# Kernel optimization log

Hardware: AMD Instinct MI355X
Metric: run time of the kernel (lower is better)

The kernel has to match this reference:

```python
import jax, jax.numpy as jnp
import numpy as np

EMB = 1024
HEADS = 16
HEAD_DIM = EMB // HEADS
EPS = 1e-5


def gelu_tanh(x):
    c = jnp.sqrt(jnp.asarray(2.0 / jnp.pi, x.dtype))
    return 0.5 * x * (1.0 + jnp.tanh(c * (x + 0.044715 * x ** 3)))


def layernorm(x, scale, shift):
    mean = jnp.mean(x, axis=-1, keepdims=True)
    var = jnp.mean((x - mean) ** 2, axis=-1, keepdims=True)  # unbiased=False
    return scale * (x - mean) / jnp.sqrt(var + EPS) + shift


def setup_inputs() -> dict:
    key = jax.random.key(0)
    ks = jax.random.split(key, 12)
    d, dff = EMB, 4 * EMB
    sd = 1.0 / np.sqrt(d)
    inp = {
        "x": jax.random.normal(ks[0], (2, 2048, d), jnp.float32),
        "Wq": jax.random.normal(ks[1], (d, d), jnp.float32) * sd,
        "Wk": jax.random.normal(ks[2], (d, d), jnp.float32) * sd,
        "Wv": jax.random.normal(ks[3], (d, d), jnp.float32) * sd,
        "Wo": jax.random.normal(ks[4], (d, d), jnp.float32) * sd,
        "bo": jnp.zeros((d,), jnp.float32),
        "W1": jax.random.normal(ks[5], (d, dff), jnp.float32) * sd,
        "b1": jnp.zeros((dff,), jnp.float32),
        "W2": jax.random.normal(ks[6], (dff, d), jnp.float32) * (1.0 / np.sqrt(dff)),
        "b2": jnp.zeros((d,), jnp.float32),
        "g1": jnp.ones((d,), jnp.float32),
        "s1": jnp.zeros((d,), jnp.float32),
        "g2": jnp.ones((d,), jnp.float32),
        "s2": jnp.zeros((d,), jnp.float32),
    }
    return inp


def attention(x, Wq, Wk, Wv, Wo, bo):
    b, s, d = x.shape
    def heads(W):
        return (x @ W).reshape(b, s, HEADS, HEAD_DIM).transpose(0, 2, 1, 3)  # b h s hd
    q, k, v = heads(Wq), heads(Wk), heads(Wv)
    scores = jnp.einsum("bhqd,bhkd->bhqk", q, k)
    causal = jnp.tril(jnp.ones((s, s), bool))
    scores = jnp.where(causal, scores, -jnp.inf)
    w = jax.nn.softmax(scores / np.sqrt(HEAD_DIM), axis=-1)
    ctx = jnp.einsum("bhqk,bhkd->bqhd", w, v).reshape(b, s, d)
    return ctx @ Wo + bo


def reference(x, Wq, Wk, Wv, Wo, bo, W1, b1, W2, b2, g1, s1, g2, s2):
    h = x + attention(layernorm(x, g1, s1), Wq, Wk, Wv, Wo, bo)
    y = layernorm(h, g2, s2)
    y = gelu_tanh(y @ W1 + b1) @ W2 + b2
    return h + y
```

## Files before the change

kernel.cpp:

```cpp
#include <hip/hip_runtime.h>
#include <hip/hip_bf16.h>
#include <stdint.h>
#include <math.h>

#define EMB   1024
#define DFF   4096
#define HEADS 16
#define HD    64
#define BATCH 2
#define SEQ   2048
#define ROWS  (BATCH * SEQ)

typedef __hip_bfloat16 bf16;
typedef short bf16x8_t __attribute__((ext_vector_type(8)));
typedef float f32x4_t __attribute__((ext_vector_type(4)));

typedef const uint32_t __attribute__((address_space(1)))* gp_t;
typedef uint32_t __attribute__((address_space(3)))* lp_t;

__device__ __forceinline__ void async_copy16(const bf16* g, short* l) {
    __builtin_amdgcn_global_load_lds((gp_t)(const void*)g, (lp_t)(void*)l, 16, 0, 0);
}

__device__ __forceinline__ void wait_lds() {
    __asm__ volatile("" ::: "memory");
    __builtin_amdgcn_s_waitcnt(0xC07F);
    __asm__ volatile("" ::: "memory");
}

__device__ __forceinline__ float gelu_f(float x) {
    float z = 0.7978845608028654f * (x + 0.044715f * x * x * x);
    float e = __builtin_amdgcn_exp2f(z * 2.885390081777927f);
    float t = 1.0f - 2.0f * __builtin_amdgcn_rcpf(e + 1.0f);
    return 0.5f * x * (1.0f + t);
}

__device__ __forceinline__ short bf16_bits(float x) {
    bf16 b = (bf16)x;
    short s;
    __builtin_memcpy(&s, &b, 2);
    return s;
}

__device__ __forceinline__ bf16x8_t load8(const bf16* p) {
    bf16x8_t v;
    __builtin_memcpy(&v, p, 16);
    return v;
}

template<int EPI, int BM>
__global__ __launch_bounds__(256) void gemm_k(
    const bf16* __restrict__ A, const bf16* __restrict__ BT,
    bf16* __restrict__ outB, float* __restrict__ outF,
    const float* __restrict__ bias, const float* __restrict__ resF,
    int N, int K, size_t bStrideZ, size_t cStrideZ)
{
    __shared__ alignas(16) short As[2][BM * 32];
    __shared__ alignas(16) short Bs[2][128 * 32];
    constexpr int AI  = BM / 32;
    constexpr int AIS = BM / 64;
    const int tid  = threadIdx.x;
    const int wave = tid >> 6;
    const int lane = tid & 63;
    const int quad = lane >> 4;
    const int l16  = lane & 15;
    const int m0 = blockIdx.y * BM;
    const int n0 = blockIdx.x * 128;
    const int wm = (wave >> 1) * (BM / 2);
    const int wn = (wave & 1) * 64;

    const bf16* Bz = BT + (size_t)blockIdx.z * bStrideZ;

    const bf16* Ag[AIS]; int aoff[AIS];
    const bf16* Bg[2];   int boff[2];
    #pragma unroll
    for (int i = 0; i < AIS; i++) {
        const int c = i * 256 + tid;
        const int row = c >> 2;
        const int lch = (c & 3) ^ ((row >> 1) & 3);
        Ag[i]   = A + (size_t)(m0 + row) * K + lch * 8;
        aoff[i] = (i * 256 + wave * 64) * 8;
    }
    #pragma unroll
    for (int i = 0; i < 2; i++) {
        const int c = i * 256 + tid;
        const int row = c >> 2;
        const int lch = (c & 3) ^ ((row >> 1) & 3);
        Bg[i]   = Bz + (size_t)(n0 + row) * K + lch * 8;
        boff[i] = (i * 256 + wave * 64) * 8;
    }

    f32x4_t acc[AI][4] = {};

    #pragma unroll
    for (int i = 0; i < AIS; i++) async_copy16(Ag[i], &As[0][aoff[i]]);
    #pragma unroll
    for (int i = 0; i < 2; i++)   async_copy16(Bg[i], &Bs[0][boff[i]]);
    __syncthreads();

    int cur = 0;
    for (int k0 = 0; k0 < K; k0 += 32) {
        const int kn = k0 + 32;
        if (kn < K) {
            #pragma unroll
            for (int i = 0; i < AIS; i++) async_copy16(Ag[i] + kn, &As[cur ^ 1][aoff[i]]);
            #pragma unroll
            for (int i = 0; i < 2; i++)   async_copy16(Bg[i] + kn, &Bs[cur ^ 1][boff[i]]);
        }
        bf16x8_t a[AI], b[4];
        #pragma unroll
        for (int i = 0; i < AI; i++) {
            const int r = wm + i * 16 + l16;
            a[i] = *(const bf16x8_t*)&As[cur][r * 32 + ((quad ^ ((r >> 1) & 3)) << 3)];
        }
        #pragma unroll
        for (int j = 0; j < 4; j++) {
            const int r = wn + j * 16 + l16;
            b[j] = *(const bf16x8_t*)&Bs[cur][r * 32 + ((quad ^ ((r >> 1) & 3)) << 3)];
        }
        #pragma unroll
        for (int i = 0; i < AI; i++)
            #pragma unroll
            for (int j = 0; j < 4; j++)
                acc[i][j] = __builtin_amdgcn_mfma_f32_16x16x32_bf16(
                    a[i], b[j], acc[i][j], 0, 0, 0);
        __syncthreads();
        cur ^= 1;
    }

    bf16* outBz = (EPI == 0) ? outB + (size_t)blockIdx.z * cStrideZ : outB;
    #pragma unroll
    for (int j = 0; j < 4; j++) {
        const int col = n0 + wn + j * 16 + l16;
        float bv = 0.0f;
        if constexpr (EPI != 0) bv = bias[col];
        #pragma unroll
        for (int i = 0; i < AI; i++) {
            #pragma unroll
            for (int r = 0; r < 4; r++) {
                const int row = m0 + wm + i * 16 + quad * 4 + r;
                float v = acc[i][j][r] + bv;
                if constexpr (EPI == 1 || EPI == 3) {
                    v += resF[(size_t)row * N + col];
                    outF[(size_t)row * N + col] = v;
                } else if constexpr (EPI == 2) {
                    outBz[(size_t)row * N + col] = (bf16)gelu_f(v);
                } else {
                    outBz[(size_t)row * N + col] = (bf16)v;
                }
            }
        }
    }
}

__global__ __launch_bounds__(256) void ln_k(
    const float* __restrict__ x, const float* __restrict__ g,
    const float* __restrict__ s, bf16* __restrict__ out)
{
    const int row = blockIdx.x;
    const int t = threadIdx.x;
    const size_t base = (size_t)row * EMB + t * 4;
    float v[4];
    #pragma unroll
    for (int e = 0; e < 4; e++) v[e] = x[base + e];
    float sum = v[0] + v[1] + v[2] + v[3];
    float sq  = v[0]*v[0] + v[1]*v[1] + v[2]*v[2] + v[3]*v[3];
    #pragma unroll
    for (int o = 1; o < 64; o <<= 1) {
        sum += __shfl_xor(sum, o);
        sq  += __shfl_xor(sq, o);
    }
    __shared__ float ssum[4], ssq[4];
    const int wave = t >> 6;
    if ((t & 63) == 0) { ssum[wave] = sum; ssq[wave] = sq; }
    __syncthreads();
    sum = ssum[0] + ssum[1] + ssum[2] + ssum[3];
    sq  = ssq[0] + ssq[1] + ssq[2] + ssq[3];
    const float mean = sum * (1.0f / EMB);
    const float var  = sq * (1.0f / EMB) - mean * mean;
    const float rstd = rsqrtf(var + 1e-5f);
    #pragma unroll
    for (int e = 0; e < 4; e++)
        out[base + e] = (bf16)(g[t * 4 + e] * (v[e] - mean) * rstd + s[t * 4 + e]);
}

template<typename T>
__global__ __launch_bounds__(256) void transpose_k(
    const T* __restrict__ src, bf16* __restrict__ dst, int R, int C)
{
    __shared__ bf16 tile[64][65];
    const size_t bo = (size_t)blockIdx.z * R * C;
    const int tx = threadIdx.x, ty = threadIdx.y;
    const int r0 = blockIdx.y * 64, c0 = blockIdx.x * 64;
    #pragma unroll
    for (int i = 0; i < 16; i++) {
        int r = ty + i * 4;
        tile[r][tx] = (bf16)(float)src[bo + (size_t)(r0 + r) * C + c0 + tx];
    }
    __syncthreads();
    #pragma unroll
    for (int i = 0; i < 16; i++) {
        int c = ty + i * 4;
        dst[bo + (size_t)(c0 + c) * R + r0 + tx] = tile[tx][c];
    }
}

__global__ __launch_bounds__(256) void transpose3_k(
    const float* __restrict__ s0, const float* __restrict__ s1,
    const float* __restrict__ s2, bf16* __restrict__ dst, int R, int C)
{
    __shared__ bf16 tile[64][65];
    const float* src = blockIdx.z == 0 ? s0 : (blockIdx.z == 1 ? s1 : s2);
    bf16* d = dst + (size_t)blockIdx.z * R * C;
    const int tx = threadIdx.x, ty = threadIdx.y;
    const int r0 = blockIdx.y * 64, c0 = blockIdx.x * 64;
    #pragma unroll
    for (int i = 0; i < 16; i++) {
        int r = ty + i * 4;
        tile[r][tx] = (bf16)src[(size_t)(r0 + r) * C + c0 + tx];
    }
    __syncthreads();
    #pragma unroll
    for (int i = 0; i < 16; i++) {
        int c = ty + i * 4;
        d[(size_t)(c0 + c) * R + r0 + tx] = tile[tx][c];
    }
}

__global__ __launch_bounds__(256) void attn_k(
    const bf16* __restrict__ q, const bf16* __restrict__ k,
    const bf16* __restrict__ vt, bf16* __restrict__ ctx)
{
    __shared__ alignas(16) short Ks[2][64 * 64];
    __shared__ alignas(16) short Vs[2][64 * 64];
    __shared__ alignas(16) short P[4][16 * 40];
    const int tid = threadIdx.x;
    const int wv = tid >> 6;
    const int lane = tid & 63;
    const int quad = lane >> 4, l16 = lane & 15;

    const int fid = (int)blockIdx.x;
    const int lid = (fid & 7) * 128 + (fid >> 3);
    const int chunk = 31 - (lid & 31);
    const int h = (lid >> 5) & 15;
    const int b = lid >> 9;
    const size_t rowBase = (size_t)b * SEQ;
    const int qb = chunk * 64 + wv * 16;
    const int NK = chunk + 1;

    const bf16* kcol  = k + rowBase * EMB + h * HD;
    const bf16* vbase = vt + (size_t)(b * HEADS + h) * HD * SEQ;

    bf16x8_t aq[2];
    #pragma unroll
    for (int s2 = 0; s2 < 2; s2++)
        aq[s2] = load8(&q[(rowBase + qb + l16) * EMB + h * HD + s2 * 32 + quad * 8]);

    f32x4_t O[4] = {};
    float l_p[4] = {};

    int krw[2], kgc[2];
    #pragma unroll
    for (int i = 0; i < 2; i++) {
        const int c = i * 256 + tid;
        krw[i] = c >> 3;
        kgc[i] = (c & 7) ^ (krw[i] & 7);
    }
    const int ldsOff[2] = { (0 * 256 + wv * 64) * 8, (1 * 256 + wv * 64) * 8 };

    #pragma unroll
    for (int i = 0; i < 2; i++) {
        async_copy16(kcol + (size_t)krw[i] * EMB + kgc[i] * 8, &Ks[0][ldsOff[i]]);
        async_copy16(vbase + (size_t)krw[i] * SEQ + kgc[i] * 8, &Vs[0][ldsOff[i]]);
    }
    __syncthreads();

    constexpr float SC = 0.125f * 1.44269504088896f;

    int cur = 0;
    for (int kb = 0; kb < NK; ++kb) {
        const int kbase = kb * 64;
        if (kb + 1 < NK) {
            const int nb = kbase + 64;
            #pragma unroll
            for (int i = 0; i < 2; i++) {
                async_copy16(kcol + (size_t)(nb + krw[i]) * EMB + kgc[i] * 8,
                             &Ks[cur ^ 1][ldsOff[i]]);
                async_copy16(vbase + (size_t)krw[i] * SEQ + nb + kgc[i] * 8,
                             &Vs[cur ^ 1][ldsOff[i]]);
            }
        }
        bf16x8_t ck[4][2];
        #pragma unroll
        for (int nt = 0; nt < 4; nt++) {
            const int kr = nt * 16 + l16;
            #pragma unroll
            for (int s2 = 0; s2 < 2; s2++)
                ck[nt][s2] = *(const bf16x8_t*)
                    &Ks[cur][kr * 64 + (((s2 * 4 + quad) ^ (kr & 7)) << 3)];
        }
        f32x4_t sc[4] = {};
        #pragma unroll
        for (int nt = 0; nt < 4; nt++)
            #pragma unroll
            for (int s2 = 0; s2 < 2; s2++)
                sc[nt] = __builtin_amdgcn_mfma_f32_16x16x32_bf16(
                    aq[s2], ck[nt][s2], sc[nt], 0, 0, 0);

        short* Pw = P[wv];
        const bool full = (kbase + 63 <= qb);
        #pragma unroll
        for (int hf = 0; hf < 2; hf++) {
            bf16x8_t cv[4];
            #pragma unroll
            for (int c = 0; c < 4; c++) {
                const int vr = c * 16 + l16;
                cv[c] = *(const bf16x8_t*)
                    &Vs[cur][vr * 64 + (((hf * 4 + quad) ^ (vr & 7)) << 3)];
            }
            if (full) {
                #pragma unroll
                for (int nt2 = 0; nt2 < 2; nt2++) {
                    const int nt = hf * 2 + nt2;
                    #pragma unroll
                    for (int r = 0; r < 4; r++) {
                        const float p = __builtin_amdgcn_exp2f(sc[nt][r] * SC);
                        l_p[r] += p;
                        Pw[(quad * 4 + r) * 40 + nt2 * 16 + l16] = bf16_bits(p);
                    }
                }
            } else {
                #pragma unroll
                for (int nt2 = 0; nt2 < 2; nt2++) {
                    const int nt = hf * 2 + nt2;
                    const int kk = kbase + nt * 16 + l16;
                    #pragma unroll
                    for (int r = 0; r < 4; r++) {
                        const int qg = qb + quad * 4 + r;
                        float s = sc[nt][r] * SC;
                        if (kk > qg) s = -1e30f;
                        const float p = __builtin_amdgcn_exp2f(s);
                        l_p[r] += p;
                        Pw[(quad * 4 + r) * 40 + nt2 * 16 + l16] = bf16_bits(p);
                    }
                }
            }
            wait_lds();
            bf16x8_t pa = *(const bf16x8_t*)&Pw[l16 * 40 + quad * 8];
            #pragma unroll
            for (int c = 0; c < 4; c++)
                O[c] = __builtin_amdgcn_mfma_f32_16x16x32_bf16(pa, cv[c], O[c], 0, 0, 0);
        }
        __syncthreads();
        cur ^= 1;
    }

    #pragma unroll
    for (int r = 0; r < 4; r++) {
        float l = l_p[r];
        l += __shfl_xor(l, 1);
        l += __shfl_xor(l, 2);
        l += __shfl_xor(l, 4);
        l += __shfl_xor(l, 8);
        const float inv = 1.0f / l;
        #pragma unroll
        for (int c = 0; c < 4; c++)
            ctx[(rowBase + qb + quad * 4 + r) * EMB + h * HD + c * 16 + l16]
                = (bf16)(O[c][r] * inv);
    }
}

extern "C" void kernel_launch(void* const* d_in, const int* in_sizes, int n_in,
                              void* d_out, int out_size, void* d_ws, size_t ws_size,
                              hipStream_t stream) {
    const float* X  = (const float*)d_in[0];
    const float* Wq = (const float*)d_in[1];
    const float* Wk = (const float*)d_in[2];
    const float* Wv = (const float*)d_in[3];
    const float* Wo = (const float*)d_in[4];
    const float* bo = (const float*)d_in[5];
    const float* W1 = (const float*)d_in[6];
    const float* b1 = (const float*)d_in[7];
    const float* W2 = (const float*)d_in[8];
    const float* b2 = (const float*)d_in[9];
    const float* g1 = (const float*)d_in[10];
    const float* s1 = (const float*)d_in[11];
    const float* g2 = (const float*)d_in[12];
    const float* s2 = (const float*)d_in[13];
    float* out = (float*)d_out;

    char* ws = (char*)d_ws;
    const size_t MB = 1024 * 1024;
    bf16*  lnbuf = (bf16*)(ws + 0);
    bf16*  qkv   = (bf16*)(ws + 8 * MB);
    bf16*  vtb   = (bf16*)(ws + 32 * MB);
    bf16*  ctx   = (bf16*)(ws + 40 * MB);
    float* hbuf  = (float*)(ws + 48 * MB);
    bf16*  WqT   = (bf16*)(ws + 64 * MB);
    bf16*  WoT   = (bf16*)(ws + 70 * MB);
    bf16*  ffn1  = (bf16*)(ws + 8 * MB);
    bf16*  W1T   = (bf16*)(ws + 40 * MB);
    bf16*  W2T   = (bf16*)(ws + 64 * MB);

    const dim3 tb(64, 4);
    transpose3_k<<<dim3(16, 16, 3), tb, 0, stream>>>(Wq, Wk, Wv, WqT, EMB, EMB);
    transpose_k<float><<<dim3(16, 16, 1), tb, 0, stream>>>(Wo, WoT, EMB, EMB);

    ln_k<<<ROWS, 256, 0, stream>>>(X, g1, s1, lnbuf);

    gemm_k<0, 128><<<dim3(8, 32, 3), 256, 0, stream>>>(
        lnbuf, WqT, qkv, nullptr, nullptr, nullptr,
        EMB, EMB, (size_t)EMB * EMB, (size_t)ROWS * EMB);

    transpose_k<bf16><<<dim3(16, 32, BATCH), tb, 0, stream>>>(
        qkv + (size_t)2 * ROWS * EMB, vtb, SEQ, EMB);

    attn_k<<<1024, 256, 0, stream>>>(
        qkv, qkv + (size_t)ROWS * EMB, vtb, ctx);

    gemm_k<1, 64><<<dim3(8, 64), 256, 0, stream>>>(
        ctx, WoT, nullptr, hbuf, bo, X, EMB, EMB, 0, 0);

    transpose_k<float><<<dim3(64, 16, 1), tb, 0, stream>>>(W1, W1T, EMB, DFF);
    transpose_k<float><<<dim3(16, 64, 1), tb, 0, stream>>>(W2, W2T, DFF, EMB);

    ln_k<<<ROWS, 256, 0, stream>>>(hbuf, g2, s2, lnbuf);

    gemm_k<2, 128><<<dim3(32, 32), 256, 0, stream>>>(
        lnbuf, W1T, ffn1, nullptr, b1, nullptr, DFF, EMB, 0, 0);

    gemm_k<3, 64><<<dim3(8, 64), 256, 0, stream>>>(
        ffn1, W2T, nullptr, out, b2, hbuf, EMB, DFF, 0, 0);
}
```

Baseline: 380.2 us.

## Interleave QKV output, add XCD-aware block remap, raise MFMA wave priority

The QKV projection now writes one interleaved [rows, 3072] buffer instead of three planar slabs. The V transpose and the attention kernel read Q, K and V from that buffer with stride 3072. The two N=1024 GEMMs (Wo and W2) now use a 1D grid with a remap that groups consecutive tiles onto the same XCD, aiming for better L2 reuse. The attention kernel also wraps its MFMA sections in s_setprio to favour waves issuing matrix ops. The strided QKV layout makes K and Q loads less contiguous per head, and the priority hints may or may not help scheduling.

```diff
diff --git a/kernel.cpp b/kernel.cpp
--- a/kernel.cpp
+++ b/kernel.cpp
@@ -4,6 +4,7 @@
 #include <math.h>
 
 #define EMB   1024
+#define QS    3072
 #define DFF   4096
 #define HEADS 16
 #define HD    64
@@ -48,12 +49,12 @@
     return v;
 }
 
-template<int EPI, int BM>
+template<int EPI, int BM, bool XCD>
 __global__ __launch_bounds__(256) void gemm_k(
     const bf16* __restrict__ A, const bf16* __restrict__ BT,
     bf16* __restrict__ outB, float* __restrict__ outF,
     const float* __restrict__ bias, const float* __restrict__ resF,
-    int N, int K, size_t bStrideZ, size_t cStrideZ)
+    int N, int K, int gx)
 {
     __shared__ alignas(16) short As[2][BM * 32];
     __shared__ alignas(16) short Bs[2][128 * 32];
@@ -64,12 +65,22 @@
     const int lane = tid & 63;
     const int quad = lane >> 4;
     const int l16  = lane & 15;
-    const int m0 = blockIdx.y * BM;
-    const int n0 = blockIdx.x * 128;
+
+    int bx, by;
+    if constexpr (XCD) {
+        const int nb  = (int)gridDim.x;
+        const int q8  = nb >> 3;
+        const int lid = ((int)blockIdx.x & 7) * q8 + ((int)blockIdx.x >> 3);
+        bx = lid % gx;
+        by = lid / gx;
+    } else {
+        bx = blockIdx.x;
+        by = blockIdx.y;
+    }
+    const int m0 = by * BM;
+    const int n0 = bx * 128;
     const int wm = (wave >> 1) * (BM / 2);
     const int wn = (wave & 1) * 64;
-
-    const bf16* Bz = BT + (size_t)blockIdx.z * bStrideZ;
 
     const bf16* Ag[AIS]; int aoff[AIS];
     const bf16* Bg[2];   int boff[2];
@@ -86,7 +97,7 @@
         const int c = i * 256 + tid;
         const int row = c >> 2;
         const int lch = (c & 3) ^ ((row >> 1) & 3);
-        Bg[i]   = Bz + (size_t)(n0 + row) * K + lch * 8;
+        Bg[i]   = BT + (size_t)(n0 + row) * K + lch * 8;
         boff[i] = (i * 256 + wave * 64) * 8;
     }
 
@@ -128,7 +139,6 @@
         cur ^= 1;
     }
 
-    bf16* outBz = (EPI == 0) ? outB + (size_t)blockIdx.z * cStrideZ : outB;
     #pragma unroll
     for (int j = 0; j < 4; j++) {
         const int col = n0 + wn + j * 16 + l16;
@@ -144,9 +154,9 @@
                     v += resF[(size_t)row * N + col];
                     outF[(size_t)row * N + col] = v;
                 } else if constexpr (EPI == 2) {
-                    outBz[(size_t)row * N + col] = (bf16)gelu_f(v);
+                    outB[(size_t)row * N + col] = (bf16)gelu_f(v);
                 } else {
-                    outBz[(size_t)row * N + col] = (bf16)v;
+                    outB[(size_t)row * N + col] = (bf16)v;
                 }
             }
         }
@@ -184,24 +194,22 @@
         out[base + e] = (bf16)(g[t * 4 + e] * (v[e] - mean) * rstd + s[t * 4 + e]);
 }
 
-template<typename T>
 __global__ __launch_bounds__(256) void transpose_k(
-    const T* __restrict__ src, bf16* __restrict__ dst, int R, int C)
+    const float* __restrict__ src, bf16* __restrict__ dst, int R, int C)
 {
     __shared__ bf16 tile[64][65];
-    const size_t bo = (size_t)blockIdx.z * R * C;
     const int tx = threadIdx.x, ty = threadIdx.y;
     const int r0 = blockIdx.y * 64, c0 = blockIdx.x * 64;
     #pragma unroll
     for (int i = 0; i < 16; i++) {
         int r = ty + i * 4;
-        tile[r][tx] = (bf16)(float)src[bo + (size_t)(r0 + r) * C + c0 + tx];
+        tile[r][tx] = (bf16)src[(size_t)(r0 + r) * C + c0 + tx];
     }
     __syncthreads();
     #pragma unroll
     for (int i = 0; i < 16; i++) {
         int c = ty + i * 4;
-        dst[bo + (size_t)(c0 + c) * R + r0 + tx] = tile[tx][c];
+        dst[(size_t)(c0 + c) * R + r0 + tx] = tile[tx][c];
     }
 }
 
@@ -227,9 +235,30 @@
     }
 }
 
+__global__ __launch_bounds__(256) void transpose_v_k(
+    const bf16* __restrict__ src, bf16* __restrict__ dst)
+{
+    __shared__ bf16 tile[64][65];
+    const int tx = threadIdx.x, ty = threadIdx.y;
+    const int r0 = blockIdx.y * 64, c0 = blockIdx.x * 64;
+    const size_t so = (size_t)blockIdx.z * SEQ * QS;
+    const size_t do_ = (size_t)blockIdx.z * EMB * SEQ;
+    #pragma unroll
+    for (int i = 0; i < 16; i++) {
+        int r = ty + i * 4;
+        tile[r][tx] = src[so + (size_t)(r0 + r) * QS + c0 + tx];
+    }
+    __syncthreads();
+    #pragma unroll
+    for (int i = 0; i < 16; i++) {
+        int c = ty + i * 4;
+        dst[do_ + (size_t)(c0 + c) * SEQ + r0 + tx] = tile[tx][c];
+    }
+}
+
 __global__ __launch_bounds__(256) void attn_k(
-    const bf16* __restrict__ q, const bf16* __restrict__ k,
-    const bf16* __restrict__ vt, bf16* __restrict__ ctx)
+    const bf16* __restrict__ qkv, const bf16* __restrict__ vt,
+    bf16* __restrict__ ctx)
 {
     __shared__ alignas(16) short Ks[2][64 * 64];
     __shared__ alignas(16) short Vs[2][64 * 64];
@@ -248,13 +277,13 @@
     const int qb = chunk * 64 + wv * 16;
     const int NK = chunk + 1;
 
-    const bf16* kcol  = k + rowBase * EMB + h * HD;
+    const bf16* kcol  = qkv + 1024 + rowBase * QS + h * HD;
     const bf16* vbase = vt + (size_t)(b * HEADS + h) * HD * SEQ;
 
     bf16x8_t aq[2];
     #pragma unroll
     for (int s2 = 0; s2 < 2; s2++)
-        aq[s2] = load8(&q[(rowBase + qb + l16) * EMB + h * HD + s2 * 32 + quad * 8]);
+        aq[s2] = load8(&qkv[(rowBase + qb + l16) * QS + h * HD + s2 * 32 + quad * 8]);
 
     f32x4_t O[4] = {};
     float l_p[4] = {};
@@ -270,7 +299,7 @@
 
     #pragma unroll
     for (int i = 0; i < 2; i++) {
-        async_copy16(kcol + (size_t)krw[i] * EMB + kgc[i] * 8, &Ks[0][ldsOff[i]]);
+        async_copy16(kcol + (size_t)krw[i] * QS + kgc[i] * 8, &Ks[0][ldsOff[i]]);
         async_copy16(vbase + (size_t)krw[i] * SEQ + kgc[i] * 8, &Vs[0][ldsOff[i]]);
     }
     __syncthreads();
@@ -284,7 +313,7 @@
             const int nb = kbase + 64;
             #pragma unroll
             for (int i = 0; i < 2; i++) {
-                async_copy16(kcol + (size_t)(nb + krw[i]) * EMB + kgc[i] * 8,
+                async_copy16(kcol + (size_t)(nb + krw[i]) * QS + kgc[i] * 8,
                              &Ks[cur ^ 1][ldsOff[i]]);
                 async_copy16(vbase + (size_t)krw[i] * SEQ + nb + kgc[i] * 8,
                              &Vs[cur ^ 1][ldsOff[i]]);
@@ -300,12 +329,14 @@
                     &Ks[cur][kr * 64 + (((s2 * 4 + quad) ^ (kr & 7)) << 3)];
         }
         f32x4_t sc[4] = {};
+        __builtin_amdgcn_s_setprio(1);
         #pragma unroll
         for (int nt = 0; nt < 4; nt++)
             #pragma unroll
             for (int s2 = 0; s2 < 2; s2++)
                 sc[nt] = __builtin_amdgcn_mfma_f32_16x16x32_bf16(
                     aq[s2], ck[nt][s2], sc[nt], 0, 0, 0);
+        __builtin_amdgcn_s_setprio(0);
 
         short* Pw = P[wv];
         const bool full = (kbase + 63 <= qb);
@@ -347,9 +378,11 @@
             }
             wait_lds();
             bf16x8_t pa = *(const bf16x8_t*)&Pw[l16 * 40 + quad * 8];
+            __builtin_amdgcn_s_setprio(1);
             #pragma unroll
             for (int c = 0; c < 4; c++)
                 O[c] = __builtin_amdgcn_mfma_f32_16x16x32_bf16(pa, cv[c], O[c], 0, 0, 0);
+            __builtin_amdgcn_s_setprio(0);
         }
         __syncthreads();
         cur ^= 1;
@@ -404,31 +437,28 @@
 
     const dim3 tb(64, 4);
     transpose3_k<<<dim3(16, 16, 3), tb, 0, stream>>>(Wq, Wk, Wv, WqT, EMB, EMB);
-    transpose_k<float><<<dim3(16, 16, 1), tb, 0, stream>>>(Wo, WoT, EMB, EMB);
+    transpose_k<<<dim3(16, 16, 1), tb, 0, stream>>>(Wo, WoT, EMB, EMB);
 
     ln_k<<<ROWS, 256, 0, stream>>>(X, g1, s1, lnbuf);
 
-    gemm_k<0, 128><<<dim3(8, 32, 3), 256, 0, stream>>>(
-        lnbuf, WqT, qkv, nullptr, nullptr, nullptr,
-        EMB, EMB, (size_t)EMB * EMB, (size_t)ROWS * EMB);
-
-    transpose_k<bf16><<<dim3(16, 32, BATCH), tb, 0, stream>>>(
-        qkv + (size_t)2 * ROWS * EMB, vtb, SEQ, EMB);
-
-    attn_k<<<1024, 256, 0, stream>>>(
-        qkv, qkv + (size_t)ROWS * EMB, vtb, ctx);
-
-    gemm_k<1, 64><<<dim3(8, 64), 256, 0, stream>>>(
-        ctx, WoT, nullptr, hbuf, bo, X, EMB, EMB, 0, 0);
-
-    transpose_k<float><<<dim3(64, 16, 1), tb, 0, stream>>>(W1, W1T, EMB, DFF);
-    transpose_k<float><<<dim3(16, 64, 1), tb, 0, stream>>>(W2, W2T, DFF, EMB);
+    gemm_k<0, 128, false><<<dim3(24, 32), 256, 0, stream>>>(
+        lnbuf, WqT, qkv, nullptr, nullptr, nullptr, QS, EMB, 0);
+
+    transpose_v_k<<<dim3(16, 32, BATCH), tb, 0, stream>>>(qkv + 2048, vtb);
+
+    attn_k<<<1024, 256, 0, stream>>>(qkv, vtb, ctx);
+
+    gemm_k<1, 64, true><<<512, 256, 0, stream>>>(
+        ctx, WoT, nullptr, hbuf, bo, X, EMB, EMB, 8);
+
+    transpose_k<<<dim3(64, 16, 1), tb, 0, stream>>>(W1, W1T, EMB, DFF);
+    transpose_k<<<dim3(16, 64, 1), tb, 0, stream>>>(W2, W2T, DFF, EMB);
 
     ln_k<<<ROWS, 256, 0, stream>>>(hbuf, g2, s2, lnbuf);
 
-    gemm_k<2, 128><<<dim3(32, 32), 256, 0, stream>>>(
-        lnbuf, W1T, ffn1, nullptr, b1, nullptr, DFF, EMB, 0, 0);
-
-    gemm_k<3, 64><<<dim3(8, 64), 256, 0, stream>>>(
-        ffn1, W2T, nullptr, out, b2, hbuf, EMB, DFF, 0, 0);
-}
+    gemm_k<2, 128, false><<<dim3(32, 32), 256, 0, stream>>>(
+        lnbuf, W1T, ffn1, nullptr, b1, nullptr, DFF, EMB, 0);
+
+    gemm_k<3, 64, true><<<512, 256, 0, stream>>>(
+        ffn1, W2T, nullptr, out, b2, hbuf, EMB, DFF, 8);
+}
```

Result: faster. 372.0 us (-2.1%).
